# Kernel optimization log

Hardware: AMD Instinct MI355X
Metric: run time of the kernel (lower is better)

The kernel has to match this reference:

```python
import jax, jax.numpy as jnp
import numpy as np

K, PS, WS, WT = 7, 7, 8, 1
NHEADS, STRIDE0, STRIDE1 = 2, 4, 1


def reflect(idx, n):
    # mirror (no edge repeat) reflection, as in stnls reflect_bounds
    idx = jnp.where(idx < 0, -idx, idx)
    idx = jnp.where(idx >= n, 2 * (n - 1) - idx, idx)
    return idx


def setup_inputs():
    key = jax.random.key(0)
    k0, k1 = jax.random.split(key)
    B, T, C, H, W = 1, 4, 64, 192, 192
    vid0 = jax.random.normal(k0, (B, T, C, H, W), jnp.float32)
    vid1 = jax.random.normal(k1, (B, T, C, H, W), jnp.float32)
    return {"vid0": vid0, "vid1": vid1}


def _search(vid0, vid1):
    B, T, C, H, W = vid0.shape
    m = NHEADS
    cph = C // m
    psh = PS // 2
    nH, nW = H // STRIDE0, W // STRIDE0
    qh = jnp.arange(nH) * STRIDE0  # query centers (stride0 grid)
    qw = jnp.arange(nW) * STRIDE0
    dy = jnp.arange(PS) - psh  # patch offsets
    h0 = reflect(qh[:, None] + dy[None, :], H)  # [nH, ps]
    w0 = reflect(qw[:, None] + dy[None, :], W)  # [nW, ps]
    # query patches: [B,T,m,cph,nH,nW,ps,ps]
    P0 = vid0[:, :, :, h0[:, None, :, None], w0[None, :, None, :]]
    P0 = P0.reshape(B, T, m, cph, nH, nW, PS, PS)

    wsh = (WS - 1) // 2
    doff = (jnp.arange(WS) - wsh) * STRIDE1  # spatial window offsets
    dts = jnp.arange(-WT, WT + 1)  # temporal window offsets
    DT, DI, DJ = jnp.meshgrid(dts, doff, doff, indexing="ij")
    offs = jnp.stack([DT.ravel(), DI.ravel(), DJ.ravel()], -1)  # [L,3]
    tbase = jnp.arange(T)

    def one_offset(off):
        dt, di, dj = off[0], off[1], off[2]
        tmap = jnp.clip(tbase + dt, 0, T - 1)  # clamp temporal window
        h1 = reflect(qh[:, None] + di + dy[None, :], H)
        w1 = reflect(qw[:, None] + dj + dy[None, :], W)
        P1 = vid1[:, tmap][:, :, :, h1[:, None, :, None], w1[None, :, None, :]]
        P1 = P1.reshape(B, T, m, cph, nH, nW, PS, PS)
        # per-head product distance (inner product over patch)
        return jnp.einsum("btmchwyx,btmchwyx->btmhw", P0, P1)

    dists_all = jax.lax.map(one_offset, offs)  # [L,B,T,m,nH,nW]
    L = offs.shape[0]
    Q = T * nH * nW
    dists_all = jnp.transpose(dists_all, (1, 3, 2, 4, 5, 0)).reshape(B, m, Q, L)
    vals, idx = jax.lax.top_k(dists_all, K)  # prod search: descending

    # candidate center coordinates per (offset, query axis)
    tc = jnp.clip(tbase[None, :] + offs[:, 0:1], 0, T - 1)  # [L,T]
    hc = reflect(qh[None, :] + offs[:, 1:2], H)  # [L,nH]
    wc = reflect(qw[None, :] + offs[:, 2:3], W)  # [L,nW]
    idxr = idx.reshape(B, m, T, nH, nW, K)
    tsel = tc[idxr, tbase[None, None, :, None, None, None]]
    hsel = hc[idxr, jnp.arange(nH)[None, None, None, :, None, None]]
    wsel = wc[idxr, jnp.arange(nW)[None, None, None, None, :, None]]
    inds = jnp.stack([tsel, hsel, wsel], -1).reshape(B, m, Q, K, 3)
    return vals, inds.astype(jnp.int32)


def reference(vid0, vid1):
    # returns (dists [B,nheads,Q,k], inds [B,nheads,Q,k,3])
    return _search(vid0, vid1)
```

## Files before the change

kernel.cpp:

```cpp
#include <hip/hip_runtime.h>


#define HH 192
#define WW 192
#define HW (HH * WW)
#define TSLICE (192 * 192 * 64)
#define ROWST  (192 * 64)
#define TVID   (4 * TSLICE)

__device__ __forceinline__ int reflect_i(int idx, int n) {
    idx = idx < 0 ? -idx : idx;
    idx = idx >= n ? 2 * (n - 1) - idx : idx;
    return idx;
}

template <int CTRL>
__device__ __forceinline__ float dpp_add(float x) {
    int y = __builtin_amdgcn_update_dpp(0, __float_as_int(x), CTRL, 0xf, 0xf, true);
    return x + __int_as_float(y);
}

__device__ __forceinline__ float reduce32(float v) {
    v = dpp_add<0x111>(v);
    v = dpp_add<0x112>(v);
    v = dpp_add<0x114>(v);
    v = dpp_add<0x118>(v);
    v = dpp_add<0x142>(v);
    return v;
}

__global__ __launch_bounds__(256) void transpose_k(
    const float* __restrict__ v0, const float* __restrict__ v1,
    float* __restrict__ ws)
{
    __shared__ float tile[64 * 65];
    const int wt  = blockIdx.x;
    const int h   = blockIdx.y;
    const int z   = blockIdx.z;
    const int vid = z >> 2;
    const int t   = z & 3;
    const int w0  = wt * 64;
    const int tid = threadIdx.x;
    const int a   = tid & 63;
    const int g   = tid >> 6;
    const float* src = (vid ? v1 : v0) + (size_t)t * 64 * HW + h * WW + w0;
    float* dst = ws + (size_t)vid * TVID + ((size_t)(t * 192 + h) * 192 + w0) * 64;
    #pragma unroll
    for (int cc = g; cc < 64; cc += 4)
        tile[cc * 65 + a] = src[(size_t)cc * HW + a];
    __syncthreads();
    #pragma unroll
    for (int ww = g; ww < 64; ww += 4)
        dst[ww * 64 + a] = tile[a * 65 + ww];
}

__global__ __launch_bounds__(256) void nls_fast(
    const float* __restrict__ T0,
    const float* __restrict__ T1,
    float* __restrict__ out)
{
    __shared__ float score[2 * 192];

    const int b    = blockIdx.x;
    const int xcd  = b & 7;
    const int loc  = b >> 3;
    const int qjp  = loc % 24;
    const int r1   = loc / 24;
    const int qi_l = r1 % 6;
    const int r2   = r1 / 6;
    const int t    = r2 & 3;
    const int hd   = r2 >> 2;
    const int qi   = xcd * 6 + qi_l;

    const int qh  = qi * 4;
    const int qw0 = qjp * 8;

    const int tid  = threadIdx.x;
    const int lane = tid & 63;
    const int wid  = tid >> 6;

    const int c     = lane & 31;
    const int hhalf = lane >> 5;
    const int q     = wid >> 1;
    const int d     = wid & 1;
    const int cg    = hd * 32 + c;
    const int qwq   = qw0 + 4 * q;

    float a[7][7];
    {
        #pragma unroll
        for (int y = 0; y < 7; ++y) {
            const int hv = reflect_i(qh - 3 + y, HH);
            const float* rp = T0 + (size_t)(t * 192 + hv) * ROWST + cg;
            #pragma unroll
            for (int x = 0; x < 7; ++x) {
                const int wv = reflect_i(qwq - 3 + x, WW);
                a[y][x] = rp[wv * 64];
            }
        }
    }

    const bool interior = (qi >= 2) && (qi <= 46) && (qjp >= 1) && (qjp <= 22);

#define FMA_BLOCK                                                        \
    {                                                                    \
        const int dlo = r > 6 ? r - 6 : 0;                               \
        const int dhi = r < 3 ? r : 3;                                   \
        _Pragma("unroll")                                                \
        for (int dip = 0; dip < 4; ++dip) {                              \
            if (dip >= dlo && dip <= dhi) {                              \
                const int y = r - dip;                                   \
                _Pragma("unroll")                                        \
                for (int djp = 0; djp < 4; ++djp) {                      \
                    _Pragma("unroll")                                    \
                    for (int x = 0; x < 7; ++x) {                        \
                        acc[dip * 4 + djp] =                             \
                            fmaf(a[y][x], rw[djp + x], acc[dip * 4 + djp]); \
                    }                                                    \
                }                                                        \
            }                                                            \
        }                                                                \
    }

    int tprev = -1;
    for (int dtI = 0; dtI < 3; ++dtI) {
        int tp = t + dtI - 1;
        tp = tp < 0 ? 0 : (tp > 3 ? 3 : tp);

        __syncthreads();

        if (tp == tprev) {
            if (tid < 128) {
                int qq = tid >> 6, o = tid & 63;
                score[qq * 192 + dtI * 64 + o] = score[qq * 192 + (dtI - 1) * 64 + o];
            }
            continue;
        }
        tprev = tp;

        float acc[16];
        #pragma unroll
        for (int k = 0; k < 16; ++k) acc[k] = 0.f;

        if (interior) {
            const float* P = T1 + (size_t)(tp * 192 + qh - 6 + 4 * d) * ROWST
                           + (qwq - 6 + 4 * hhalf) * 64 + cg;
            #pragma unroll
            for (int r = 0; r < 10; ++r) {
                const float* pr = P + r * ROWST;
                float rw[10];
                #pragma unroll
                for (int v = 0; v < 10; ++v) rw[v] = pr[v * 64];
                FMA_BLOCK
            }
        } else {
            int wo[10];
            #pragma unroll
            for (int v = 0; v < 10; ++v)
                wo[v] = reflect_i(qwq - 6 + 4 * hhalf + v, WW) * 64 + cg;
            const float* Pt = T1 + (size_t)tp * TSLICE;
            #pragma unroll
            for (int r = 0; r < 10; ++r) {
                const int hv = reflect_i(qh - 6 + 4 * d + r, HH);
                const float* pr = Pt + (size_t)hv * ROWST;
                float rw[10];
                #pragma unroll
                for (int v = 0; v < 10; ++v) rw[v] = pr[wo[v]];
                FMA_BLOCK
            }
        }

        #pragma unroll
        for (int k = 0; k < 16; ++k) acc[k] = reduce32(acc[k]);

        if ((lane & 31) == 31) {
            float* sp = &score[q * 192 + dtI * 64 + 4 * hhalf];
            #pragma unroll
            for (int dip = 0; dip < 4; ++dip)
                #pragma unroll
                for (int djp = 0; djp < 4; ++djp)
                    sp[(4 * d + dip) * 8 + djp] = acc[dip * 4 + djp];
        }
    }
#undef FMA_BLOCK

    __syncthreads();

    if (wid < 2) {
        const int qq = wid;
        const int qj = 2 * qjp + qq;
        float v0 = score[qq * 192 + lane];
        float v1 = score[qq * 192 + 64 + lane];
        float v2 = score[qq * 192 + 128 + lane];
        const int qglob = (t * 48 + qi) * 48 + qj;
        const int vbase = (hd * 9216 + qglob) * 7;
        const int ibase = 129024 + vbase * 3;
        for (int r = 0; r < 7; ++r) {
            float bv = v0; int bi = lane;
            if (v1 > bv) { bv = v1; bi = lane + 64; }
            if (v2 > bv) { bv = v2; bi = lane + 128; }
            #pragma unroll
            for (int m = 1; m <= 32; m <<= 1) {
                float ov = __shfl_xor(bv, m);
                int   oi = __shfl_xor(bi, m);
                if (ov > bv || (ov == bv && oi < bi)) { bv = ov; bi = oi; }
            }
            if (lane == 0) {
                out[vbase + r] = bv;
                int dtSel = bi >> 6;
                int rr    = bi & 63;
                int diSel = (rr >> 3) - 3;
                int djSel = (rr & 7) - 3;
                int ts = t + dtSel - 1;
                ts = ts < 0 ? 0 : (ts > 3 ? 3 : ts);
                int hs = reflect_i(qh + diSel, HH);
                int ws = reflect_i(qj * 4 + djSel, WW);
                float* op = out + ibase + 3 * r;
                op[0] = (float)ts;
                op[1] = (float)hs;
                op[2] = (float)ws;
            }
            if ((bi & 63) == lane) {
                int slot = bi >> 6;
                if (slot == 0)      v0 = -3.4e38f;
                else if (slot == 1) v1 = -3.4e38f;
                else                v2 = -3.4e38f;
            }
        }
    }
}

#define BS_CSTR 282
#define BS_SZ   (32 * BS_CSTR)
#define AS_CSTR 86

__global__ __launch_bounds__(256) void nls_kernel(
    const float* __restrict__ vid0,
    const float* __restrict__ vid1,
    float* __restrict__ out)
{
    __shared__ float smem[BS_SZ + 2 * 192];
    float* Bs = smem;
    float* As = smem;
    float* score = smem + BS_SZ;

    const int b    = blockIdx.x;
    const int xcd  = b & 7;
    const int loc  = b >> 3;
    const int qjp  = loc % 24;
    const int r1   = loc / 24;
    const int qi_l = r1 % 6;
    const int r2   = r1 / 6;
    const int t    = r2 & 3;
    const int hd   = r2 >> 2;
    const int qi   = xcd * 6 + qi_l;

    const int qh  = qi * 4;
    const int qw0 = qjp * 8;

    const int tid  = threadIdx.x;
    const int lane = tid & 63;
    const int wid  = tid >> 6;

    const bool intA = (qi >= 1) && (qjp >= 1) && (qjp <= 22);
    const bool intB = (qi >= 2) && (qi <= 46) && (qjp >= 1) && (qjp <= 22);

    if (intA) {
        const int sc = tid & 31;
        const int gg = tid >> 5;
        const float* src = vid0 + (size_t)(t * 64 + hd * 32 + sc) * HW
                         + (qh - 3) * WW + (qw0 - 3);
        float* dstc = As + sc * AS_CSTR;
        for (int it = gg; it < 21; it += 8) {
            int u = it / 3, grp = it - u * 3;
            float4 val = *(const float4*)(src + u * WW + 4 * grp);
            float* dp = dstc + u * 12 + 4 * grp;
            *(float2*)(dp)     = make_float2(val.x, val.y);
            *(float2*)(dp + 2) = make_float2(val.z, val.w);
        }
    } else {
        const int sc = tid >> 3;
        const int vl = tid & 7;
        const float* src = vid0 + (size_t)(t * 64 + hd * 32 + sc) * HW;
        const int wa0 = reflect_i(qw0 - 3 + vl, WW);
        const int wa1 = (vl < 4) ? reflect_i(qw0 + 5 + vl, WW) : 0;
        float* dst = As + sc * AS_CSTR + vl;
        #pragma unroll
        for (int u = 0; u < 7; ++u) {
            int hh = reflect_i(qh - 3 + u, HH);
            const float* rp = src + hh * WW;
            dst[u * 12] = rp[wa0];
            if (vl < 4) dst[u * 12 + 8] = rp[wa1];
        }
    }
    __syncthreads();

    const int c     = lane & 31;
    const int hhalf = lane >> 5;
    const int q     = wid >> 1;
    const int d     = wid & 1;

    float a[7][8];
    {
        const float* Ab = As + c * AS_CSTR + 4 * q;
        #pragma unroll
        for (int y = 0; y < 7; ++y) {
            #pragma unroll
            for (int j = 0; j < 4; ++j)
                *(float2*)&a[y][2 * j] = *(const float2*)(Ab + y * 12 + 2 * j);
        }
    }

    const float* Bc = Bs + c * BS_CSTR + (4 * d) * 20 + 4 * q + 4 * hhalf;

    int tprev = -1;
    for (int dtI = 0; dtI < 3; ++dtI) {
        int tp = t + dtI - 1;
        tp = tp < 0 ? 0 : (tp > 3 ? 3 : tp);
        __syncthreads();
        if (tp == tprev) {
            if (tid < 128) {
                int qq = tid >> 6, o = tid & 63;
                score[qq * 192 + dtI * 64 + o] = score[qq * 192 + (dtI - 1) * 64 + o];
            }
            continue;
        }
        tprev = tp;

        if (intB) {
            const int sc = tid & 31;
            const int gg = tid >> 5;
            const float* src = vid1 + (size_t)(tp * 64 + hd * 32 + sc) * HW
                             + (qh - 6) * WW + (qw0 - 6);
            float* dstc = Bs + sc * BS_CSTR;
            for (int it = gg; it < 70; it += 8) {
                int u = it / 5, grp = it - u * 5;
                float4 val = *(const float4*)(src + u * WW + 4 * grp);
                float* dp = dstc + u * 20 + 4 * grp;
                *(float2*)(dp)     = make_float2(val.x, val.y);
                *(float2*)(dp + 2) = make_float2(val.z, val.w);
            }
        } else {
            const int sc = tid >> 3;
            const int vl = tid & 7;
            const float* src = vid1 + (size_t)(tp * 64 + hd * 32 + sc) * HW;
            const int w0 = reflect_i(qw0 - 6 + vl, WW);
            const int w1 = reflect_i(qw0 + 2 + vl, WW);
            const int w2 = (vl < 4) ? reflect_i(qw0 + 10 + vl, WW) : 0;
            float* dst = Bs + sc * BS_CSTR + vl;
            #pragma unroll
            for (int u = 0; u < 14; ++u) {
                int hh2 = reflect_i(qh - 6 + u, HH);
                const float* rp = src + hh2 * WW;
                dst[u * 20]     = rp[w0];
                dst[u * 20 + 8] = rp[w1];
                if (vl < 4) dst[u * 20 + 16] = rp[w2];
            }
        }
        __syncthreads();

        {
            float acc[16];
            #pragma unroll
            for (int k = 0; k < 16; ++k) acc[k] = 0.f;
            #pragma unroll
            for (int r = 0; r < 10; ++r) {
                float rw[12];
                const float* Br = Bc + r * 20;
                #pragma unroll
                for (int j = 0; j < 6; ++j)
                    *(float2*)&rw[2 * j] = *(const float2*)(Br + 2 * j);
                const int dlo = r > 6 ? r - 6 : 0;
                const int dhi = r < 3 ? r : 3;
                #pragma unroll
                for (int dip = 0; dip < 4; ++dip) {
                    if (dip >= dlo && dip <= dhi) {
                        const int y = r - dip;
                        #pragma unroll
                        for (int djp = 0; djp < 4; ++djp)
                            #pragma unroll
                            for (int x = 0; x < 7; ++x)
                                acc[dip * 4 + djp] =
                                    fmaf(a[y][x], rw[djp + x], acc[dip * 4 + djp]);
                    }
                }
            }
            #pragma unroll
            for (int k = 0; k < 16; ++k) acc[k] = reduce32(acc[k]);
            if ((lane & 31) == 31) {
                float* sp = &score[q * 192 + dtI * 64 + 4 * hhalf];
                #pragma unroll
                for (int dip = 0; dip < 4; ++dip) {
                    float* dp = sp + (4 * d + dip) * 8;
                    *(float2*)(dp)     = make_float2(acc[dip * 4 + 0], acc[dip * 4 + 1]);
                    *(float2*)(dp + 2) = make_float2(acc[dip * 4 + 2], acc[dip * 4 + 3]);
                }
            }
        }
    }

    __syncthreads();

    if (wid < 2) {
        const int qq = wid;
        const int qj = 2 * qjp + qq;
        float v0 = score[qq * 192 + lane];
        float v1 = score[qq * 192 + 64 + lane];
        float v2 = score[qq * 192 + 128 + lane];
        const int qglob = (t * 48 + qi) * 48 + qj;
        const int vbase = (hd * 9216 + qglob) * 7;
        const int ibase = 129024 + vbase * 3;
        for (int r = 0; r < 7; ++r) {
            float bv = v0; int bi = lane;
            if (v1 > bv) { bv = v1; bi = lane + 64; }
            if (v2 > bv) { bv = v2; bi = lane + 128; }
            #pragma unroll
            for (int m = 1; m <= 32; m <<= 1) {
                float ov = __shfl_xor(bv, m);
                int   oi = __shfl_xor(bi, m);
                if (ov > bv || (ov == bv && oi < bi)) { bv = ov; bi = oi; }
            }
            if (lane == 0) {
                out[vbase + r] = bv;
                int dtSel = bi >> 6;
                int rr    = bi & 63;
                int diSel = (rr >> 3) - 3;
                int djSel = (rr & 7) - 3;
                int ts = t + dtSel - 1;
                ts = ts < 0 ? 0 : (ts > 3 ? 3 : ts);
                int hs = reflect_i(qh + diSel, HH);
                int ws = reflect_i(qj * 4 + djSel, WW);
                float* op = out + ibase + 3 * r;
                op[0] = (float)ts;
                op[1] = (float)hs;
                op[2] = (float)ws;
            }
            if ((bi & 63) == lane) {
                int slot = bi >> 6;
                if (slot == 0)      v0 = -3.4e38f;
                else if (slot == 1) v1 = -3.4e38f;
                else                v2 = -3.4e38f;
            }
        }
    }
}

extern "C" void kernel_launch(void* const* d_in, const int* in_sizes, int n_in,
                              void* d_out, int out_size, void* d_ws, size_t ws_size,
                              hipStream_t stream) {
    const float* vid0 = (const float*)d_in[0];
    const float* vid1 = (const float*)d_in[1];
    float* out = (float*)d_out;
    const size_t need = 2ull * (size_t)TVID * sizeof(float);
    if (ws_size >= need) {
        float* ws = (float*)d_ws;
        transpose_k<<<dim3(3, 192, 8), 256, 0, stream>>>(vid0, vid1, ws);
        nls_fast<<<dim3(9216), 256, 0, stream>>>(ws, ws + TVID, out);
    } else {
        nls_kernel<<<dim3(9216), 256, 0, stream>>>(vid0, vid1, out);
    }
}
```

Measured before the change: 339.6 us.

## Transpose only vid1; stage query patches from NCHW vid0 through LDS

The transpose kernel now converts only vid1 to channel-last layout, which halves its read/write traffic and workspace. The fast search kernel loads the 7x11 query window for 32 channels directly from the original vid0 into shared memory, then builds the per-thread patch registers from LDS. The time loop is fully unrolled and the extra barrier plus score copy for repeated clamped time frames are gone; scores for a repeated frame are rewritten from the retained accumulators. The cost is an extra barrier at kernel start and uncoalesced strided vid0 reads in the staging step.

```diff
diff --git a/kernel.cpp b/kernel.cpp
--- a/kernel.cpp
+++ b/kernel.cpp
@@ -7,6 +7,8 @@
 #define TSLICE (192 * 192 * 64)
 #define ROWST  (192 * 64)
 #define TVID   (4 * TSLICE)
+
+#define AS_CSTR 79
 
 __device__ __forceinline__ int reflect_i(int idx, int n) {
     idx = idx < 0 ? -idx : idx;
@@ -30,21 +32,18 @@
 }
 
 __global__ __launch_bounds__(256) void transpose_k(
-    const float* __restrict__ v0, const float* __restrict__ v1,
-    float* __restrict__ ws)
+    const float* __restrict__ v1, float* __restrict__ ws)
 {
     __shared__ float tile[64 * 65];
     const int wt  = blockIdx.x;
     const int h   = blockIdx.y;
-    const int z   = blockIdx.z;
-    const int vid = z >> 2;
-    const int t   = z & 3;
+    const int t   = blockIdx.z;
     const int w0  = wt * 64;
     const int tid = threadIdx.x;
     const int a   = tid & 63;
     const int g   = tid >> 6;
-    const float* src = (vid ? v1 : v0) + (size_t)t * 64 * HW + h * WW + w0;
-    float* dst = ws + (size_t)vid * TVID + ((size_t)(t * 192 + h) * 192 + w0) * 64;
+    const float* src = v1 + (size_t)t * 64 * HW + h * WW + w0;
+    float* dst = ws + ((size_t)(t * 192 + h) * 192 + w0) * 64;
     #pragma unroll
     for (int cc = g; cc < 64; cc += 4)
         tile[cc * 65 + a] = src[(size_t)cc * HW + a];
@@ -55,10 +54,11 @@
 }
 
 __global__ __launch_bounds__(256) void nls_fast(
-    const float* __restrict__ T0,
+    const float* __restrict__ vid0,
     const float* __restrict__ T1,
     float* __restrict__ out)
 {
+    __shared__ float As[32 * AS_CSTR];
     __shared__ float score[2 * 192];
 
     const int b    = blockIdx.x;
@@ -79,6 +79,21 @@
     const int lane = tid & 63;
     const int wid  = tid >> 6;
 
+    {
+        const int sc = tid >> 3;
+        const int vl = tid & 7;
+        if (vl < 7) {
+            const float* src = vid0 + (size_t)(t * 64 + hd * 32 + sc) * HW;
+            const int hh = reflect_i(qh - 3 + vl, HH);
+            const float* rp = src + hh * WW;
+            float* dst = As + sc * AS_CSTR + vl * 11;
+            #pragma unroll
+            for (int x = 0; x < 11; ++x)
+                dst[x] = rp[reflect_i(qw0 - 3 + x, WW)];
+        }
+    }
+    __syncthreads();
+
     const int c     = lane & 31;
     const int hhalf = lane >> 5;
     const int q     = wid >> 1;
@@ -88,16 +103,12 @@
 
     float a[7][7];
     {
+        const float* Ab = As + c * AS_CSTR + 4 * q;
         #pragma unroll
-        for (int y = 0; y < 7; ++y) {
-            const int hv = reflect_i(qh - 3 + y, HH);
-            const float* rp = T0 + (size_t)(t * 192 + hv) * ROWST + cg;
-            #pragma unroll
-            for (int x = 0; x < 7; ++x) {
-                const int wv = reflect_i(qwq - 3 + x, WW);
-                a[y][x] = rp[wv * 64];
-            }
-        }
+        for (int y = 0; y < 7; ++y)
+            #pragma unroll
+            for (int x = 0; x < 7; ++x)
+                a[y][x] = Ab[y * 11 + x];
     }
 
     const bool interior = (qi >= 2) && (qi <= 46) && (qjp >= 1) && (qjp <= 22);
@@ -122,56 +133,49 @@
         }                                                                \
     }
 
+    float acc[16];
     int tprev = -1;
+    #pragma unroll
     for (int dtI = 0; dtI < 3; ++dtI) {
         int tp = t + dtI - 1;
         tp = tp < 0 ? 0 : (tp > 3 ? 3 : tp);
 
-        __syncthreads();
-
-        if (tp == tprev) {
-            if (tid < 128) {
-                int qq = tid >> 6, o = tid & 63;
-                score[qq * 192 + dtI * 64 + o] = score[qq * 192 + (dtI - 1) * 64 + o];
-            }
-            continue;
-        }
-        tprev = tp;
-
-        float acc[16];
-        #pragma unroll
-        for (int k = 0; k < 16; ++k) acc[k] = 0.f;
-
-        if (interior) {
-            const float* P = T1 + (size_t)(tp * 192 + qh - 6 + 4 * d) * ROWST
-                           + (qwq - 6 + 4 * hhalf) * 64 + cg;
-            #pragma unroll
-            for (int r = 0; r < 10; ++r) {
-                const float* pr = P + r * ROWST;
-                float rw[10];
-                #pragma unroll
-                for (int v = 0; v < 10; ++v) rw[v] = pr[v * 64];
-                FMA_BLOCK
-            }
-        } else {
-            int wo[10];
-            #pragma unroll
-            for (int v = 0; v < 10; ++v)
-                wo[v] = reflect_i(qwq - 6 + 4 * hhalf + v, WW) * 64 + cg;
-            const float* Pt = T1 + (size_t)tp * TSLICE;
-            #pragma unroll
-            for (int r = 0; r < 10; ++r) {
-                const int hv = reflect_i(qh - 6 + 4 * d + r, HH);
-                const float* pr = Pt + (size_t)hv * ROWST;
-                float rw[10];
-                #pragma unroll
-                for (int v = 0; v < 10; ++v) rw[v] = pr[wo[v]];
-                FMA_BLOCK
-            }
-        }
-
-        #pragma unroll
-        for (int k = 0; k < 16; ++k) acc[k] = reduce32(acc[k]);
+        if (tp != tprev) {
+            tprev = tp;
+            #pragma unroll
+            for (int k = 0; k < 16; ++k) acc[k] = 0.f;
+
+            if (interior) {
+                const float* P = T1 + (size_t)(tp * 192 + qh - 6 + 4 * d) * ROWST
+                               + (qwq - 6 + 4 * hhalf) * 64 + cg;
+                #pragma unroll
+                for (int r = 0; r < 10; ++r) {
+                    const float* pr = P + r * ROWST;
+                    float rw[10];
+                    #pragma unroll
+                    for (int v = 0; v < 10; ++v) rw[v] = pr[v * 64];
+                    FMA_BLOCK
+                }
+            } else {
+                int wo[10];
+                #pragma unroll
+                for (int v = 0; v < 10; ++v)
+                    wo[v] = reflect_i(qwq - 6 + 4 * hhalf + v, WW) * 64 + cg;
+                const float* Pt = T1 + (size_t)tp * TSLICE;
+                #pragma unroll
+                for (int r = 0; r < 10; ++r) {
+                    const int hv = reflect_i(qh - 6 + 4 * d + r, HH);
+                    const float* pr = Pt + (size_t)hv * ROWST;
+                    float rw[10];
+                    #pragma unroll
+                    for (int v = 0; v < 10; ++v) rw[v] = pr[wo[v]];
+                    FMA_BLOCK
+                }
+            }
+
+            #pragma unroll
+            for (int k = 0; k < 16; ++k) acc[k] = reduce32(acc[k]);
+        }
 
         if ((lane & 31) == 31) {
             float* sp = &score[q * 192 + dtI * 64 + 4 * hhalf];
@@ -232,7 +236,7 @@
 
 #define BS_CSTR 282
 #define BS_SZ   (32 * BS_CSTR)
-#define AS_CSTR 86
+#define AF_CSTR 86
 
 __global__ __launch_bounds__(256) void nls_kernel(
     const float* __restrict__ vid0,
@@ -241,7 +245,7 @@
 {
     __shared__ float smem[BS_SZ + 2 * 192];
     float* Bs = smem;
-    float* As = smem;
+    float* Asf = smem;
     float* score = smem + BS_SZ;
 
     const int b    = blockIdx.x;
@@ -270,7 +274,7 @@
         const int gg = tid >> 5;
         const float* src = vid0 + (size_t)(t * 64 + hd * 32 + sc) * HW
                          + (qh - 3) * WW + (qw0 - 3);
-        float* dstc = As + sc * AS_CSTR;
+        float* dstc = Asf + sc * AF_CSTR;
         for (int it = gg; it < 21; it += 8) {
             int u = it / 3, grp = it - u * 3;
             float4 val = *(const float4*)(src + u * WW + 4 * grp);
@@ -284,7 +288,7 @@
         const float* src = vid0 + (size_t)(t * 64 + hd * 32 + sc) * HW;
         const int wa0 = reflect_i(qw0 - 3 + vl, WW);
         const int wa1 = (vl < 4) ? reflect_i(qw0 + 5 + vl, WW) : 0;
-        float* dst = As + sc * AS_CSTR + vl;
+        float* dst = Asf + sc * AF_CSTR + vl;
         #pragma unroll
         for (int u = 0; u < 7; ++u) {
             int hh = reflect_i(qh - 3 + u, HH);
@@ -302,7 +306,7 @@
 
     float a[7][8];
     {
-        const float* Ab = As + c * AS_CSTR + 4 * q;
+        const float* Ab = Asf + c * AF_CSTR + 4 * q;
         #pragma unroll
         for (int y = 0; y < 7; ++y) {
             #pragma unroll
@@ -451,11 +455,11 @@
     const float* vid0 = (const float*)d_in[0];
     const float* vid1 = (const float*)d_in[1];
     float* out = (float*)d_out;
-    const size_t need = 2ull * (size_t)TVID * sizeof(float);
+    const size_t need = (size_t)TVID * sizeof(float);
     if (ws_size >= need) {
         float* ws = (float*)d_ws;
-        transpose_k<<<dim3(3, 192, 8), 256, 0, stream>>>(vid0, vid1, ws);
-        nls_fast<<<dim3(9216), 256, 0, stream>>>(ws, ws + TVID, out);
+        transpose_k<<<dim3(3, 192, 4), 256, 0, stream>>>(vid1, ws);
+        nls_fast<<<dim3(9216), 256, 0, stream>>>(vid0, ws, out);
     } else {
         nls_kernel<<<dim3(9216), 256, 0, stream>>>(vid0, vid1, out);
     }
```

Result: slower. 351.2 us (+3.4%).
